# Kernel optimization log

Measured on AMD Instinct MI355X. Metric: run time of the kernel, lower is better.

The kernel has to match this reference:

```python
import jax, jax.numpy as jnp
import numpy as np

NUM_CUSTOMERS = 300000
NUM_PRODUCTS = 150000
NUM_GROUPS = 2000
NUM_BRANDS = 500
EMB_DIM = 64
NUM_LAYERS = 3


def setup_inputs() -> dict:
    key = jax.random.key(0)
    ks = jax.random.split(key, 20)
    def ri(k, n, hi):
        return jax.random.randint(k, (n,), 0, hi, dtype=jnp.int32)
    return {
        'cust_w': 0.1 * jax.random.normal(ks[0], (NUM_CUSTOMERS, EMB_DIM), jnp.float32),
        'prod_w': 0.1 * jax.random.normal(ks[1], (NUM_PRODUCTS, EMB_DIM), jnp.float32),
        'group_w': 0.1 * jax.random.normal(ks[2], (NUM_GROUPS, EMB_DIM), jnp.float32),
        'brand_w': 0.1 * jax.random.normal(ks[3], (NUM_BRANDS, EMB_DIM), jnp.float32),
        'purch_src': ri(ks[4], 2000000, NUM_CUSTOMERS),
        'purch_dst': ri(ks[5], 2000000, NUM_PRODUCTS),
        'pby_src': ri(ks[6], 2000000, NUM_PRODUCTS),
        'pby_dst': ri(ks[7], 2000000, NUM_CUSTOMERS),
        'sim_src': ri(ks[8], 500000, NUM_PRODUCTS),
        'sim_dst': ri(ks[9], 500000, NUM_PRODUCTS),
        'cop_src': ri(ks[10], 1000000, NUM_PRODUCTS),
        'cop_dst': ri(ks[11], 1000000, NUM_PRODUCTS),
        'bel_src': ri(ks[12], 150000, NUM_PRODUCTS),
        'bel_dst': ri(ks[13], 150000, NUM_GROUPS),
        'comp_src': ri(ks[14], 300000, NUM_PRODUCTS),
        'comp_dst': ri(ks[15], 300000, NUM_BRANDS),
    }


def _propagate(src_idx, tgt_idx, tgt_emb, n_src):
    # gather target embeddings along edges, scatter-add into source buckets,
    # normalize by source out-degree (clamped to >= 1) -- LightGCN mean-agg.
    msg = tgt_emb[tgt_idx]                                    # [E, D]
    agg = jax.ops.segment_sum(msg, src_idx, num_segments=n_src)
    cnt = jax.ops.segment_sum(jnp.ones(src_idx.shape, tgt_emb.dtype),
                              src_idx, num_segments=n_src)
    return agg / jnp.maximum(cnt, 1.0)[:, None]


def reference(cust_w, prod_w, group_w, brand_w,
              purch_src, purch_dst, pby_src, pby_dst,
              sim_src, sim_dst, cop_src, cop_dst,
              bel_src, bel_dst, comp_src, comp_dst):
    customer_emb, product_emb = cust_w, prod_w
    group_emb, brand_emb = group_w, brand_w
    customer_embs = [customer_emb]
    product_embs = [product_emb]
    for _ in range(NUM_LAYERS):
        customer_to_product = _propagate(purch_src, purch_dst, product_emb, NUM_CUSTOMERS)
        product_agg = product_emb
        product_agg = product_agg + _propagate(pby_src, pby_dst, customer_emb, NUM_PRODUCTS)
        product_agg = product_agg + 0.5 * _propagate(sim_src, sim_dst, product_emb, NUM_PRODUCTS)
        product_agg = product_agg + 0.3 * _propagate(cop_src, cop_dst, product_emb, NUM_PRODUCTS)
        product_agg = product_agg + 0.2 * _propagate(bel_src, bel_dst, group_emb, NUM_PRODUCTS)
        product_agg = product_agg + 0.2 * _propagate(comp_src, comp_dst, brand_emb, NUM_PRODUCTS)
        customer_emb = customer_to_product
        product_emb = product_agg
        customer_embs.append(customer_emb)
        product_embs.append(product_emb)
    final_customer = jnp.mean(jnp.stack(customer_embs, 0), axis=0)
    final_product = jnp.mean(jnp.stack(product_embs, 0), axis=0)
    # group/brand embeddings are never updated -> mean of identical copies
    return (final_customer, final_product, group_emb, brand_emb)
```

## Files before the change

kernel.cpp:

```cpp
#include <hip/hip_runtime.h>

#define NC 300000
#define NP 150000
#define NG 2000
#define NB 500
#define SCAN_B 1024
#define BK_SHIFT 11
#define BK_KEYS 2048
#define CBASE (NC + 1)
#define RTOT (CBASE + 5 * NP + 1)
#define NBKT 513
#define CH 8192
#define ROWS (NP + NC)
#define RCH 4096

typedef unsigned int u32;
typedef float  f32x4 __attribute__((ext_vector_type(4)));
typedef unsigned int u32x4 __attribute__((ext_vector_type(4)));

static inline unsigned cdiv(long long a, long long b) { return (unsigned)((a + b - 1) / b); }

__device__ __forceinline__ float b2f(u32 h) {
    union { u32 u; float f; } c; c.u = h << 16; return c.f;
}
__device__ __forceinline__ u32 f2b(float f) {
    union { float f; u32 u; } c; c.f = f;
    return (c.u + 0x7FFFu + ((c.u >> 16) & 1u)) >> 16;
}
__device__ __forceinline__ void unpack8(uint4 v, float* o) {
    o[0] = b2f(v.x & 0xFFFFu); o[1] = b2f(v.x >> 16);
    o[2] = b2f(v.y & 0xFFFFu); o[3] = b2f(v.y >> 16);
    o[4] = b2f(v.z & 0xFFFFu); o[5] = b2f(v.z >> 16);
    o[6] = b2f(v.w & 0xFFFFu); o[7] = b2f(v.w >> 16);
}
__device__ __forceinline__ void unpack8v(u32x4 v, float* o) {
    o[0] = b2f(v.x & 0xFFFFu); o[1] = b2f(v.x >> 16);
    o[2] = b2f(v.y & 0xFFFFu); o[3] = b2f(v.y >> 16);
    o[4] = b2f(v.z & 0xFFFFu); o[5] = b2f(v.z >> 16);
    o[6] = b2f(v.w & 0xFFFFu); o[7] = b2f(v.w >> 16);
}
__device__ __forceinline__ uint4 pack8(const float* a) {
    uint4 v;
    v.x = f2b(a[0]) | (f2b(a[1]) << 16);
    v.y = f2b(a[2]) | (f2b(a[3]) << 16);
    v.z = f2b(a[4]) | (f2b(a[5]) << 16);
    v.w = f2b(a[6]) | (f2b(a[7]) << 16);
    return v;
}

__global__ void convert_all(const float* __restrict__ cw, const float* __restrict__ pw,
                            const float* __restrict__ gw, const float* __restrict__ bw,
                            uint4* __restrict__ c16, uint4* __restrict__ p16,
                            uint4* __restrict__ g16, uint4* __restrict__ b16,
                            float* __restrict__ outg, float* __restrict__ outb) {
    const int C8 = NC * 8, P8 = NP * 8, G8 = NG * 8, B8 = NB * 8;
    int i = blockIdx.x * blockDim.x + threadIdx.x;
    const float* in; uint4* out16; float* cpy = nullptr; int j;
    if (i < C8)                         { in = cw; out16 = c16; j = i; }
    else if ((j = i - C8) < P8)         { in = pw; out16 = p16; }
    else if ((j = i - C8 - P8) < G8)    { in = gw; out16 = g16; cpy = outg; }
    else if ((j = i - C8 - P8 - G8) < B8){ in = bw; out16 = b16; cpy = outb; }
    else return;
    const float4* p = (const float4*)(in + (size_t)j * 8);
    float4 a = p[0], b = p[1];
    float t[8] = { a.x, a.y, a.z, a.w, b.x, b.y, b.z, b.w };
    out16[j] = pack8(t);
    if (cpy) { float4* q = (float4*)(cpy + (size_t)j * 8); q[0] = a; q[1] = b; }
}

struct Edges6 {
    const int* src[6];
    const int* dst[6];
    int cum[7];
};

__device__ __forceinline__ int edge_key(int k, int src) {
    return (k == 0) ? src : CBASE + src * 5 + (k - 1);
}

__global__ void bcount(Edges6 e, int* __restrict__ gcount, int total) {
    __shared__ int hist[NBKT];
    int t = threadIdx.x;
    int j0 = blockIdx.x * CH;
    for (int b = t; b < NBKT; b += blockDim.x) hist[b] = 0;
    __syncthreads();
    #pragma unroll 4
    for (int q = 0; q < CH / 256; ++q) {
        int j = j0 + q * 256 + t;
        if (j < total) {
            int k = 0;
            #pragma unroll
            for (int qq = 1; qq < 6; ++qq) k += (j >= e.cum[qq]);
            int key = edge_key(k, __builtin_nontemporal_load(e.src[k] + (j - e.cum[k])));
            atomicAdd(&hist[key >> BK_SHIFT], 1);
        }
    }
    __syncthreads();
    for (int b = t; b < NBKT; b += blockDim.x) {
        int c = hist[b];
        if (c > 0) atomicAdd(gcount + b, c);
    }
}

__global__ void bscan(const int* __restrict__ gcount, int* __restrict__ gbase,
                      int* __restrict__ gcur, int nb) {
    __shared__ int sm[SCAN_B];
    int t = threadIdx.x;
    int v = (t < nb) ? gcount[t] : 0;
    sm[t] = v; __syncthreads();
    for (int off = 1; off < SCAN_B; off <<= 1) {
        int add = (t >= off) ? sm[t - off] : 0;
        __syncthreads();
        sm[t] += add; __syncthreads();
    }
    int excl = sm[t] - v;
    if (t < nb) { gbase[t] = excl; gcur[t] = excl; }
    if (t == nb - 1) gbase[nb] = sm[t];
}

__global__ void msplit(Edges6 e, int* __restrict__ gcur, u32* __restrict__ stage, int total) {
    __shared__ int hist[NBKT];
    __shared__ int bse[NBKT];
    int t = threadIdx.x;
    int j0 = blockIdx.x * CH;
    for (int b = t; b < NBKT; b += blockDim.x) hist[b] = 0;
    __syncthreads();
    #pragma unroll 4
    for (int q = 0; q < CH / 256; ++q) {
        int j = j0 + q * 256 + t;
        if (j < total) {
            int k = 0;
            #pragma unroll
            for (int qq = 1; qq < 6; ++qq) k += (j >= e.cum[qq]);
            int key = edge_key(k, __builtin_nontemporal_load(e.src[k] + (j - e.cum[k])));
            atomicAdd(&hist[key >> BK_SHIFT], 1);
        }
    }
    __syncthreads();
    for (int b = t; b < NBKT; b += blockDim.x) {
        int c = hist[b];
        bse[b] = (c > 0) ? atomicAdd(gcur + b, c) : 0;
        hist[b] = 0;
    }
    __syncthreads();
    #pragma unroll 4
    for (int q = 0; q < CH / 256; ++q) {
        int j = j0 + q * 256 + t;
        if (j < total) {
            int k = 0;
            #pragma unroll
            for (int qq = 1; qq < 6; ++qq) k += (j >= e.cum[qq]);
            int jj = j - e.cum[k];
            int key = edge_key(k, __builtin_nontemporal_load(e.src[k] + jj));
            int d = __builtin_nontemporal_load(e.dst[k] + jj);
            int b = key >> BK_SHIFT;
            int off = atomicAdd(&hist[b], 1);
            stage[bse[b] + off] = ((u32)(key & (BK_KEYS - 1)) << 19) | (u32)d;
        }
    }
}

__global__ void sortb(const int* __restrict__ gbase, const u32* __restrict__ stage,
                      int* __restrict__ pm, int* __restrict__ rp, int rtot) {
    __shared__ int cur[BK_KEYS];
    __shared__ int part[512];
    int b = blockIdx.x, t = threadIdx.x;
    int k0 = b << BK_SHIFT;
    int base = gbase[b], end = gbase[b + 1];
    for (int q = t; q < BK_KEYS; q += 512) cur[q] = 0;
    __syncthreads();
    for (int i = base + t; i < end; i += 512)
        atomicAdd(&cur[stage[i] >> 19], 1);
    __syncthreads();
    int a0 = cur[4 * t], a1 = cur[4 * t + 1], a2 = cur[4 * t + 2], a3 = cur[4 * t + 3];
    int s = a0 + a1 + a2 + a3;
    part[t] = s; __syncthreads();
    for (int off = 1; off < 512; off <<= 1) {
        int add = (t >= off) ? part[t - off] : 0;
        __syncthreads();
        part[t] += add; __syncthreads();
    }
    int c0 = base + part[t] - s;
    int c1 = c0 + a0, c2 = c1 + a1, c3 = c2 + a2;
    cur[4 * t] = c0; cur[4 * t + 1] = c1; cur[4 * t + 2] = c2; cur[4 * t + 3] = c3;
    int ki = k0 + 4 * t;
    if (ki + 3 < rtot) {
        *(int4*)(rp + ki) = make_int4(c0, c1, c2, c3);
    } else {
        if (ki     < rtot) rp[ki]     = c0;
        if (ki + 1 < rtot) rp[ki + 1] = c1;
        if (ki + 2 < rtot) rp[ki + 2] = c2;
        if (ki + 3 < rtot) rp[ki + 3] = c3;
    }
    __syncthreads();
    for (int i = base + t; i < end; i += 512) {
        u32 w = stage[i];
        int off = atomicAdd(&cur[w >> 19], 1);
        pm[off] = (int)(w & 0x7FFFFu);
    }
}

__device__ __forceinline__ int row_bin(const int* __restrict__ rp, int gid) {
    if (gid < NP) {
        int o = CBASE + gid * 5;
        int td = rp[o + 5] - rp[o];
        return td < 127 ? td : 127;
    } else {
        int r = gid - NP;
        int d = rp[r + 1] - rp[r];
        return 128 + (d < 127 ? d : 127);
    }
}

__global__ void rowhist(const int* __restrict__ rp, int* __restrict__ gbinc, int rows) {
    __shared__ int hist[256];
    int t = threadIdx.x;
    hist[t] = 0;
    __syncthreads();
    int j0 = blockIdx.x * RCH;
    for (int q = 0; q < RCH / 256; ++q) {
        int j = j0 + q * 256 + t;
        if (j < rows) atomicAdd(&hist[row_bin(rp, j)], 1);
    }
    __syncthreads();
    int c = hist[t];
    if (c > 0) atomicAdd(gbinc + t, c);
}

__global__ void rowscan(const int* __restrict__ gbinc, int* __restrict__ gcur256) {
    __shared__ int sm[256];
    int t = threadIdx.x;
    int v = gbinc[t];
    sm[t] = v; __syncthreads();
    for (int off = 1; off < 256; off <<= 1) {
        int add = (t >= off) ? sm[t - off] : 0;
        __syncthreads();
        sm[t] += add; __syncthreads();
    }
    gcur256[t] = sm[t] - v;
}

__global__ void rowplace(const int* __restrict__ rp, int* __restrict__ gcur256,
                         int* __restrict__ perm, int rows) {
    __shared__ int hist[256];
    __shared__ int bse[256];
    int t = threadIdx.x;
    hist[t] = 0;
    __syncthreads();
    int j0 = blockIdx.x * RCH;
    for (int q = 0; q < RCH / 256; ++q) {
        int j = j0 + q * 256 + t;
        if (j < rows) atomicAdd(&hist[row_bin(rp, j)], 1);
    }
    __syncthreads();
    int c = hist[t];
    bse[t] = (c > 0) ? atomicAdd(gcur256 + t, c) : 0;
    hist[t] = 0;
    __syncthreads();
    for (int q = 0; q < RCH / 256; ++q) {
        int j = j0 + q * 256 + t;
        if (j < rows) {
            int b = row_bin(rp, j);
            int off = atomicAdd(&hist[b], 1);
            perm[bse[b] + off] = j;
        }
    }
}

__global__ void permrp(const int* __restrict__ rp, const int* __restrict__ perm,
                       int4* __restrict__ pA, int2* __restrict__ pC,
                       int2* __restrict__ cinfo, int rows) {
    int j = blockIdx.x * blockDim.x + threadIdx.x;
    if (j >= rows) return;
    int pg = perm[j];
    if (pg < NP) {
        const int* r0 = rp + CBASE + pg * 5;
        pA[j] = make_int4(r0[0], r0[1], r0[2], r0[3]);
        pC[j] = make_int2(r0[4], r0[5]);
    } else {
        int r = pg - NP;
        cinfo[j - NP] = make_int2(rp[r], rp[r + 1]);
    }
}

__device__ __forceinline__ void acc8(uint4 v, float* sum) {
    float t[8]; unpack8(v, t);
    #pragma unroll
    for (int k = 0; k < 8; ++k) sum[k] += t[k];
}
__device__ __forceinline__ void agg8se(int s, int e, const int* __restrict__ pm,
                                       const uint4* __restrict__ tgt,
                                       int lane, float* acc) {
    float sum[8] = {0, 0, 0, 0, 0, 0, 0, 0};
    int i = s;
    for (; i + 4 <= e; i += 4) {
        int d0 = pm[i], d1 = pm[i + 1], d2 = pm[i + 2], d3 = pm[i + 3];
        uint4 v0 = tgt[(size_t)d0 * 8 + lane];
        uint4 v1 = tgt[(size_t)d1 * 8 + lane];
        uint4 v2 = tgt[(size_t)d2 * 8 + lane];
        uint4 v3 = tgt[(size_t)d3 * 8 + lane];
        acc8(v0, sum); acc8(v1, sum); acc8(v2, sum); acc8(v3, sum);
    }
    for (; i < e; ++i) {
        uint4 v = tgt[(size_t)pm[i] * 8 + lane];
        acc8(v, sum);
    }
    int deg = e - s;
    float sc = 1.0f / (float)(deg > 1 ? deg : 1);
    #pragma unroll
    for (int k = 0; k < 8; ++k) acc[k] += sum[k] * sc;
}

__device__ __forceinline__ const uint4* tblsel(int i, int b1, int b3, int b4,
                                               const uint4* c16, const uint4* p16,
                                               const uint4* g16, const uint4* b16) {
    const uint4* t = c16;
    if (i >= b1) t = p16;
    if (i >= b3) t = g16;
    if (i >= b4) t = b16;
    return t;
}
__device__ __forceinline__ float sclsel(int i, int b1, int b2, int b3, int b4,
                                        float s0, float s1, float s2, float s3, float s4) {
    float s = s0;
    if (i >= b1) s = s1;
    if (i >= b2) s = s2;
    if (i >= b3) s = s3;
    if (i >= b4) s = s4;
    return s;
}
__device__ __forceinline__ void accw(uint4 v, float s, float* acc) {
    float t[8]; unpack8(v, t);
    #pragma unroll
    for (int k = 0; k < 8; ++k) acc[k] += t[k] * s;
}

__global__ void layer_kernel(
    const int* __restrict__ perm,
    const int4* __restrict__ pA, const int2* __restrict__ pC,
    const int2* __restrict__ cinfo,
    const int* __restrict__ pm,
    const uint4* __restrict__ c16, const uint4* __restrict__ p16,
    const uint4* __restrict__ g16, const uint4* __restrict__ b16,
    uint4* __restrict__ c16n, uint4* __restrict__ p16n,
    const float* __restrict__ cw, const float* __restrict__ pw,
    const uint4* __restrict__ s1c, const uint4* __restrict__ s1p,
    float* __restrict__ outc, float* __restrict__ outp,
    int mode)
{
    int t = blockIdx.x * blockDim.x + threadIdx.x;
    int gid = t >> 3;
    int lane = t & 7;
    float acc[8];
    if (gid < NP) {
        int row = perm[gid];
        size_t idx = (size_t)row * 8 + lane;
        int4 ia = pA[gid];
        int2 ic = pC[gid];
        int b0 = ia.x, b1 = ia.y, b2 = ia.z, b3 = ia.w, b4 = ic.x, b5 = ic.y;
        int d0g = b1 - b0, d1g = b2 - b1, d2g = b3 - b2, d3g = b4 - b3, d4g = b5 - b4;
        float s0 = 1.0f / (float)(d0g > 1 ? d0g : 1);
        float s1 = 0.5f / (float)(d1g > 1 ? d1g : 1);
        float s2 = 0.3f / (float)(d2g > 1 ? d2g : 1);
        float s3 = 0.2f / (float)(d3g > 1 ? d3g : 1);
        float s4 = 0.2f / (float)(d4g > 1 ? d4g : 1);
        float base[8]; unpack8(p16[idx], base);
        #pragma unroll
        for (int k = 0; k < 8; ++k) acc[k] = base[k];
        int i = b0;
        for (; i + 4 <= b5; i += 4) {
            int e0 = pm[i], e1 = pm[i + 1], e2 = pm[i + 2], e3 = pm[i + 3];
            const uint4* t0 = tblsel(i,     b1, b3, b4, c16, p16, g16, b16);
            const uint4* t1 = tblsel(i + 1, b1, b3, b4, c16, p16, g16, b16);
            const uint4* t2 = tblsel(i + 2, b1, b3, b4, c16, p16, g16, b16);
            const uint4* t3 = tblsel(i + 3, b1, b3, b4, c16, p16, g16, b16);
            float w0 = sclsel(i,     b1, b2, b3, b4, s0, s1, s2, s3, s4);
            float w1 = sclsel(i + 1, b1, b2, b3, b4, s0, s1, s2, s3, s4);
            float w2 = sclsel(i + 2, b1, b2, b3, b4, s0, s1, s2, s3, s4);
            float w3 = sclsel(i + 3, b1, b2, b3, b4, s0, s1, s2, s3, s4);
            uint4 v0 = t0[(size_t)e0 * 8 + lane];
            uint4 v1 = t1[(size_t)e1 * 8 + lane];
            uint4 v2 = t2[(size_t)e2 * 8 + lane];
            uint4 v3 = t3[(size_t)e3 * 8 + lane];
            accw(v0, w0, acc); accw(v1, w1, acc); accw(v2, w2, acc); accw(v3, w3, acc);
        }
        for (; i < b5; ++i) {
            int e0 = pm[i];
            const uint4* t0 = tblsel(i, b1, b3, b4, c16, p16, g16, b16);
            float w0 = sclsel(i, b1, b2, b3, b4, s0, s1, s2, s3, s4);
            uint4 v0 = t0[(size_t)e0 * 8 + lane];
            accw(v0, w0, acc);
        }
        if (mode != 2) {
            p16n[idx] = pack8(acc);
        } else {
            const f32x4* s0p = (const f32x4*)(pw + (size_t)row * 64 + lane * 8);
            f32x4 a0 = __builtin_nontemporal_load(s0p);
            f32x4 a1 = __builtin_nontemporal_load(s0p + 1);
            u32x4 s1v = __builtin_nontemporal_load((const u32x4*)&s1p[idx]);
            float sv[8]; unpack8v(s1v, sv);
            f32x4 o0, o1;
            o0.x = 0.25f * (a0.x + sv[0] + base[0] + acc[0]);
            o0.y = 0.25f * (a0.y + sv[1] + base[1] + acc[1]);
            o0.z = 0.25f * (a0.z + sv[2] + base[2] + acc[2]);
            o0.w = 0.25f * (a0.w + sv[3] + base[3] + acc[3]);
            o1.x = 0.25f * (a1.x + sv[4] + base[4] + acc[4]);
            o1.y = 0.25f * (a1.y + sv[5] + base[5] + acc[5]);
            o1.z = 0.25f * (a1.z + sv[6] + base[6] + acc[6]);
            o1.w = 0.25f * (a1.w + sv[7] + base[7] + acc[7]);
            f32x4* o = (f32x4*)(outp + (size_t)row * 64 + lane * 8);
            __builtin_nontemporal_store(o0, o);
            __builtin_nontemporal_store(o1, o + 1);
        }
    } else if (gid < ROWS) {
        int row = perm[gid] - NP;
        size_t idx = (size_t)row * 8 + lane;
        int2 se = cinfo[gid - NP];
        #pragma unroll
        for (int k = 0; k < 8; ++k) acc[k] = 0.f;
        agg8se(se.x, se.y, pm, p16, lane, acc);
        if (mode != 2) {
            c16n[idx] = pack8(acc);
        } else {
            float base[8]; unpack8(c16[idx], base);
            const f32x4* s0c = (const f32x4*)(cw + (size_t)row * 64 + lane * 8);
            f32x4 a0 = __builtin_nontemporal_load(s0c);
            f32x4 a1 = __builtin_nontemporal_load(s0c + 1);
            u32x4 s1v = __builtin_nontemporal_load((const u32x4*)&s1c[idx]);
            float sv[8]; unpack8v(s1v, sv);
            f32x4 o0, o1;
            o0.x = 0.25f * (a0.x + sv[0] + base[0] + acc[0]);
            o0.y = 0.25f * (a0.y + sv[1] + base[1] + acc[1]);
            o0.z = 0.25f * (a0.z + sv[2] + base[2] + acc[2]);
            o0.w = 0.25f * (a0.w + sv[3] + base[3] + acc[3]);
            o1.x = 0.25f * (a1.x + sv[4] + base[4] + acc[4]);
            o1.y = 0.25f * (a1.y + sv[5] + base[5] + acc[5]);
            o1.z = 0.25f * (a1.z + sv[6] + base[6] + acc[6]);
            o1.w = 0.25f * (a1.w + sv[7] + base[7] + acc[7]);
            f32x4* o = (f32x4*)(outc + (size_t)row * 64 + lane * 8);
            __builtin_nontemporal_store(o0, o);
            __builtin_nontemporal_store(o1, o + 1);
        }
    }
}

extern "C" void kernel_launch(void* const* d_in, const int* in_sizes, int n_in,
                              void* d_out, int out_size, void* d_ws, size_t ws_size,
                              hipStream_t stream) {
    const float* cust_w  = (const float*)d_in[0];
    const float* prod_w  = (const float*)d_in[1];
    const float* group_w = (const float*)d_in[2];
    const float* brand_w = (const float*)d_in[3];

    const int n_purch = in_sizes[4];
    const int n_pby   = in_sizes[6];
    const int n_sim   = in_sizes[8];
    const int n_cop   = in_sizes[10];
    const int n_bel   = in_sizes[12];
    const int n_comp  = in_sizes[14];
    const int n_edges[6] = { n_purch, n_pby, n_sim, n_cop, n_bel, n_comp };

    const size_t CSZ = (size_t)NC * 64;
    const size_t PSZ = (size_t)NP * 64;

    char* base = (char*)d_ws;
    uint4* c16A = (uint4*)base;                 base += (size_t)NC * 128;
    uint4* c16B = (uint4*)base;                 base += (size_t)NC * 128;
    uint4* p16A = (uint4*)base;                 base += (size_t)NP * 128;
    uint4* p16B = (uint4*)base;                 base += (size_t)NP * 128;
    uint4* g16  = (uint4*)base;                 base += (size_t)NG * 128;
    uint4* b16  = (uint4*)base;                 base += (size_t)NB * 128;

    int* rp_all = (int*)base;                   base += (size_t)RTOT * 4;
    long long tot_edges = 0;
    for (int k = 0; k < 6; ++k) tot_edges += n_edges[k];
    int* pm_all = (int*)base;                   base += tot_edges * 4;
    u32* stage  = (u32*)base;                   base += tot_edges * 4;
    int* gcount = (int*)base;                   base += (size_t)NBKT * 4;
    int* gbase  = (int*)base;                   base += (size_t)(NBKT + 1) * 4;
    int* gcur   = (int*)base;                   base += (size_t)NBKT * 4;
    int* gbinc  = (int*)base;                   base += 256 * 4;
    int* gcur256= (int*)base;                   base += 256 * 4;
    int* perm   = (int*)base;                   base += (size_t)ROWS * 4;
    int4* pA    = (int4*)base;                  base += (size_t)NP * 16;
    int2* pC    = (int2*)base;                  base += (size_t)NP * 8;
    int2* cinfo = (int2*)base;                  base += (size_t)NC * 8;

    float* out_c = (float*)d_out;
    float* out_p = out_c + CSZ;
    float* out_g = out_p + PSZ;
    float* out_b = out_g + (size_t)NG * 64;

    const int BT = 256;

    const long long CVT = (long long)(NC + NP + NG + NB) * 8;
    convert_all<<<cdiv(CVT, BT), BT, 0, stream>>>(
        cust_w, prod_w, group_w, brand_w, c16A, p16A, g16, b16, out_g, out_b);

    Edges6 E;
    E.src[0] = (const int*)d_in[4];  E.dst[0] = (const int*)d_in[5];
    E.src[1] = (const int*)d_in[6];  E.dst[1] = (const int*)d_in[7];
    E.src[2] = (const int*)d_in[8];  E.dst[2] = (const int*)d_in[9];
    E.src[3] = (const int*)d_in[10]; E.dst[3] = (const int*)d_in[11];
    E.src[4] = (const int*)d_in[12]; E.dst[4] = (const int*)d_in[13];
    E.src[5] = (const int*)d_in[14]; E.dst[5] = (const int*)d_in[15];
    E.cum[0] = 0;
    for (int k = 0; k < 6; ++k) E.cum[k + 1] = E.cum[k] + n_edges[k];
    const int TOT = E.cum[6];

    hipMemsetAsync(gcount, 0, (size_t)NBKT * 4, stream);
    hipMemsetAsync(gbinc, 0, 256 * 4, stream);
    bcount<<<cdiv(TOT, CH), BT, 0, stream>>>(E, gcount, TOT);
    bscan<<<1, SCAN_B, 0, stream>>>(gcount, gbase, gcur, NBKT);
    msplit<<<cdiv(TOT, CH), BT, 0, stream>>>(E, gcur, stage, TOT);
    sortb<<<NBKT, 512, 0, stream>>>(gbase, stage, pm_all, rp_all, RTOT);

    rowhist<<<cdiv(ROWS, RCH), 256, 0, stream>>>(rp_all, gbinc, ROWS);
    rowscan<<<1, 256, 0, stream>>>(gbinc, gcur256);
    rowplace<<<cdiv(ROWS, RCH), 256, 0, stream>>>(rp_all, gcur256, perm, ROWS);
    permrp<<<cdiv(ROWS, BT), BT, 0, stream>>>(rp_all, perm, pA, pC, cinfo, ROWS);

    const long long LTHREADS = (long long)ROWS * 8;
    layer_kernel<<<cdiv(LTHREADS, BT), BT, 0, stream>>>(
        perm, pA, pC, cinfo, pm_all,
        c16A, p16A, g16, b16, c16B, p16B,
        cust_w, prod_w, c16B, p16B, out_c, out_p, 0);
    layer_kernel<<<cdiv(LTHREADS, BT), BT, 0, stream>>>(
        perm, pA, pC, cinfo, pm_all,
        c16B, p16B, g16, b16, c16A, p16A,
        cust_w, prod_w, c16B, p16B, out_c, out_p, 1);
    layer_kernel<<<cdiv(LTHREADS, BT), BT, 0, stream>>>(
        perm, pA, pC, cinfo, pm_all,
        c16A, p16A, g16, b16, c16B, p16B,
        cust_w, prod_w, c16B, p16B,
        out_c, out_p, 2);
}
```

Baseline: 679.6 us.

## Fuse embedding conversion into bucket count and reuse per-block histograms in split

```diff
diff --git a/kernel.cpp b/kernel.cpp
--- a/kernel.cpp
+++ b/kernel.cpp
@@ -48,26 +48,6 @@
     return v;
 }
 
-__global__ void convert_all(const float* __restrict__ cw, const float* __restrict__ pw,
-                            const float* __restrict__ gw, const float* __restrict__ bw,
-                            uint4* __restrict__ c16, uint4* __restrict__ p16,
-                            uint4* __restrict__ g16, uint4* __restrict__ b16,
-                            float* __restrict__ outg, float* __restrict__ outb) {
-    const int C8 = NC * 8, P8 = NP * 8, G8 = NG * 8, B8 = NB * 8;
-    int i = blockIdx.x * blockDim.x + threadIdx.x;
-    const float* in; uint4* out16; float* cpy = nullptr; int j;
-    if (i < C8)                         { in = cw; out16 = c16; j = i; }
-    else if ((j = i - C8) < P8)         { in = pw; out16 = p16; }
-    else if ((j = i - C8 - P8) < G8)    { in = gw; out16 = g16; cpy = outg; }
-    else if ((j = i - C8 - P8 - G8) < B8){ in = bw; out16 = b16; cpy = outb; }
-    else return;
-    const float4* p = (const float4*)(in + (size_t)j * 8);
-    float4 a = p[0], b = p[1];
-    float t[8] = { a.x, a.y, a.z, a.w, b.x, b.y, b.z, b.w };
-    out16[j] = pack8(t);
-    if (cpy) { float4* q = (float4*)(cpy + (size_t)j * 8); q[0] = a; q[1] = b; }
-}
-
 struct Edges6 {
     const int* src[6];
     const int* dst[6];
@@ -78,10 +58,33 @@
     return (k == 0) ? src : CBASE + src * 5 + (k - 1);
 }
 
-__global__ void bcount(Edges6 e, int* __restrict__ gcount, int total) {
+__global__ void conv_bcount(const float* __restrict__ cw, const float* __restrict__ pw,
+                            const float* __restrict__ gw, const float* __restrict__ bw,
+                            uint4* __restrict__ c16, uint4* __restrict__ p16,
+                            uint4* __restrict__ g16, uint4* __restrict__ b16,
+                            float* __restrict__ outg, float* __restrict__ outb,
+                            Edges6 e, int* __restrict__ gcount, int* __restrict__ bhist,
+                            int total, int nconv) {
     __shared__ int hist[NBKT];
     int t = threadIdx.x;
-    int j0 = blockIdx.x * CH;
+    if ((int)blockIdx.x < nconv) {
+        const int C8 = NC * 8, P8 = NP * 8, G8 = NG * 8, B8 = NB * 8;
+        int i = blockIdx.x * blockDim.x + t;
+        const float* in; uint4* out16; float* cpy = nullptr; int j;
+        if (i < C8)                          { in = cw; out16 = c16; j = i; }
+        else if ((j = i - C8) < P8)          { in = pw; out16 = p16; }
+        else if ((j = i - C8 - P8) < G8)     { in = gw; out16 = g16; cpy = outg; }
+        else if ((j = i - C8 - P8 - G8) < B8){ in = bw; out16 = b16; cpy = outb; }
+        else return;
+        const float4* p = (const float4*)(in + (size_t)j * 8);
+        float4 a = p[0], b = p[1];
+        float tv[8] = { a.x, a.y, a.z, a.w, b.x, b.y, b.z, b.w };
+        out16[j] = pack8(tv);
+        if (cpy) { float4* q = (float4*)(cpy + (size_t)j * 8); q[0] = a; q[1] = b; }
+        return;
+    }
+    int blk = blockIdx.x - nconv;
+    int j0 = blk * CH;
     for (int b = t; b < NBKT; b += blockDim.x) hist[b] = 0;
     __syncthreads();
     #pragma unroll 4
@@ -96,8 +99,10 @@
         }
     }
     __syncthreads();
+    int* bh = bhist + (size_t)blk * NBKT;
     for (int b = t; b < NBKT; b += blockDim.x) {
         int c = hist[b];
+        bh[b] = c;
         if (c > 0) atomicAdd(gcount + b, c);
     }
 }
@@ -118,27 +123,15 @@
     if (t == nb - 1) gbase[nb] = sm[t];
 }
 
-__global__ void msplit(Edges6 e, int* __restrict__ gcur, u32* __restrict__ stage, int total) {
+__global__ void msplit(Edges6 e, int* __restrict__ gcur, const int* __restrict__ bhist,
+                       u32* __restrict__ stage, int total) {
     __shared__ int hist[NBKT];
     __shared__ int bse[NBKT];
     int t = threadIdx.x;
     int j0 = blockIdx.x * CH;
-    for (int b = t; b < NBKT; b += blockDim.x) hist[b] = 0;
-    __syncthreads();
-    #pragma unroll 4
-    for (int q = 0; q < CH / 256; ++q) {
-        int j = j0 + q * 256 + t;
-        if (j < total) {
-            int k = 0;
-            #pragma unroll
-            for (int qq = 1; qq < 6; ++qq) k += (j >= e.cum[qq]);
-            int key = edge_key(k, __builtin_nontemporal_load(e.src[k] + (j - e.cum[k])));
-            atomicAdd(&hist[key >> BK_SHIFT], 1);
-        }
-    }
-    __syncthreads();
+    const int* bh = bhist + (size_t)blockIdx.x * NBKT;
     for (int b = t; b < NBKT; b += blockDim.x) {
-        int c = hist[b];
+        int c = bh[b];
         bse[b] = (c > 0) ? atomicAdd(gcur + b, c) : 0;
         hist[b] = 0;
     }
@@ -476,6 +469,8 @@
     for (int k = 0; k < 6; ++k) tot_edges += n_edges[k];
     int* pm_all = (int*)base;                   base += tot_edges * 4;
     u32* stage  = (u32*)base;                   base += tot_edges * 4;
+    const int NEDGE = cdiv(tot_edges, CH);
+    int* bhist  = (int*)base;                   base += (size_t)NEDGE * NBKT * 4;
     int* gcount = (int*)base;                   base += (size_t)NBKT * 4;
     int* gbase  = (int*)base;                   base += (size_t)(NBKT + 1) * 4;
     int* gcur   = (int*)base;                   base += (size_t)NBKT * 4;
@@ -492,10 +487,6 @@
     float* out_b = out_g + (size_t)NG * 64;
 
     const int BT = 256;
-
-    const long long CVT = (long long)(NC + NP + NG + NB) * 8;
-    convert_all<<<cdiv(CVT, BT), BT, 0, stream>>>(
-        cust_w, prod_w, group_w, brand_w, c16A, p16A, g16, b16, out_g, out_b);
 
     Edges6 E;
     E.src[0] = (const int*)d_in[4];  E.dst[0] = (const int*)d_in[5];
@@ -510,9 +501,15 @@
 
     hipMemsetAsync(gcount, 0, (size_t)NBKT * 4, stream);
     hipMemsetAsync(gbinc, 0, 256 * 4, stream);
-    bcount<<<cdiv(TOT, CH), BT, 0, stream>>>(E, gcount, TOT);
+
+    const long long CVT = (long long)(NC + NP + NG + NB) * 8;
+    const int NCONV = cdiv(CVT, BT);
+    conv_bcount<<<NCONV + NEDGE, BT, 0, stream>>>(
+        cust_w, prod_w, group_w, brand_w, c16A, p16A, g16, b16, out_g, out_b,
+        E, gcount, bhist, TOT, NCONV);
+
     bscan<<<1, SCAN_B, 0, stream>>>(gcount, gbase, gcur, NBKT);
-    msplit<<<cdiv(TOT, CH), BT, 0, stream>>>(E, gcur, stage, TOT);
+    msplit<<<NEDGE, BT, 0, stream>>>(E, gcur, bhist, stage, TOT);
     sortb<<<NBKT, 512, 0, stream>>>(gbase, stage, pm_all, rp_all, RTOT);
 
     rowhist<<<cdiv(ROWS, RCH), 256, 0, stream>>>(rp_all, gbinc, ROWS);
```

Measured after the change: 672.5 us. Within noise of the previous version (-1.0%).
